# Kernel optimization log

Measured on AMD Instinct MI355X. Metric: run time of the kernel, lower is better.

## Reference

```python
import jax, jax.numpy as jnp
import numpy as np

B, S, D, H, DH, W, V, K = 2, 4096, 768, 12, 64, 128, 50265, 128
NEG = -1e9


def _ln(x, g, b, eps=1e-5):
    m = jnp.mean(x, axis=-1, keepdims=True)
    v = jnp.var(x, axis=-1, keepdims=True)
    return (x - m) * jax.lax.rsqrt(v + eps) * g + b


def _split_heads(x):  # [B,S,D] -> [B,H,S,DH]
    return x.reshape(B, S, H, DH).transpose(0, 2, 1, 3)


def _windows(xc):  # [B,H,C,W,DH] -> [B,H,C,3W,DH] (prev/self/next chunk)
    xp = jnp.pad(xc, ((0, 0), (0, 0), (1, 1), (0, 0), (0, 0)))
    return jnp.concatenate([xp[:, :, :-2], xp[:, :, 1:-1], xp[:, :, 2:]], axis=3)


def _forward(sentences, start_pieces, end_pieces, labels,
             emb, pos, ln0_g, ln0_b, wq, bq, wk, bk, wv, bv, wo, bo,
             ln1_g, ln1_b, w1, b1, w2, b2, ln2_g, ln2_b, exemplars):
    C = S // W
    scale = 1.0 / np.sqrt(DH)
    am = sentences != 1  # pad token id is 1 (mask = sentence_tokens != 1)
    gidx = jnp.concatenate([start_pieces, end_pieces], axis=1)  # [B,2] global tokens
    G = gidx.shape[1]

    # embeddings
    x = _ln(emb[sentences] + pos[None], ln0_g, ln0_b)  # [B,S,D]

    # --- Longformer layer: sliding-window + global attention ---
    q = _split_heads(x @ wq + bq)
    k = _split_heads(x @ wk + bk)
    v = _split_heads(x @ wv + bv)

    qc = q.reshape(B, H, C, W, DH)
    kw = _windows(k.reshape(B, H, C, W, DH))  # [B,H,C,3W,DH]
    vw = _windows(v.reshape(B, H, C, W, DH))

    # banded local scores
    sb = jnp.einsum('bhcqd,bhckd->bhcqk', qc, kw) * scale  # [B,H,C,W,3W]
    qi = jnp.arange(W)[:, None]
    kj = jnp.arange(3 * W)[None, :]
    band = jnp.abs(kj - W - qi) <= W  # [W,3W]
    amc = jnp.pad(am.reshape(B, C, W), ((0, 0), (1, 1), (0, 0)))
    amw = jnp.concatenate([amc[:, :-2], amc[:, 1:-1], amc[:, 2:]], axis=2)  # [B,C,3W]
    mask = band[None, None, None] & amw[:, None, :, None, :]
    sb = jnp.where(mask, sb, NEG).reshape(B, H, S, 3 * W)

    # every token also attends to the G global tokens
    gk = jnp.take_along_axis(k, gidx[:, None, :, None], axis=2)  # [B,H,G,DH]
    gv = jnp.take_along_axis(v, gidx[:, None, :, None], axis=2)
    sg = jnp.einsum('bhsd,bhgd->bhsg', q, gk) * scale  # [B,H,S,G]

    p = jax.nn.softmax(jnp.concatenate([sb, sg], axis=-1), axis=-1)
    pb = p[..., :3 * W].reshape(B, H, C, W, 3 * W)
    pg = p[..., 3 * W:]
    o = jnp.einsum('bhcqk,bhckd->bhcqd', pb, vw).reshape(B, H, S, DH)
    o = o + jnp.einsum('bhsg,bhgd->bhsd', pg, gv)

    # global query tokens attend to everything
    qg = jnp.take_along_axis(q, gidx[:, None, :, None], axis=2)  # [B,H,G,DH]
    sgq = jnp.einsum('bhgd,bhsd->bhgs', qg, k) * scale
    sgq = jnp.where(am[:, None, None, :], sgq, NEG)
    og = jnp.einsum('bhgs,bhsd->bhgd', jax.nn.softmax(sgq, axis=-1), v)

    o = o.transpose(0, 2, 1, 3).reshape(B, S, D)
    og = og.transpose(0, 2, 1, 3).reshape(B, G, D)
    o = o.at[jnp.arange(B)[:, None], gidx].set(og)

    x = _ln(x + (o @ wo + bo), ln1_g, ln1_b)
    ff = jax.nn.gelu(x @ w1 + b1, approximate=False) @ w2 + b2
    h = _ln(x + ff, ln2_g, ln2_b)  # last_hidden_state

    # mention reps: gather start & end piece vectors, concat -> [B, 2D]
    sv = jnp.take_along_axis(h, start_pieces[:, :, None], axis=1)[:, 0]
    ev = jnp.take_along_axis(h, end_pieces[:, :, None], axis=1)[:, 0]
    mention = jnp.concatenate([sv, ev], axis=-1)  # [B, 1536]

    logits = mention @ exemplars.T  # [B, K]
    logp = jax.nn.log_softmax(logits, axis=-1)
    loss = -jnp.sum(jnp.take_along_axis(logp, labels[:, None], axis=1))
    return logits, loss


def setup_inputs() -> dict:
    key = jax.random.key(0)
    ks = jax.random.split(key, 16)
    f = lambda k, s: (jax.random.normal(k, s, dtype=jnp.float32) * 0.02)
    return {
        'sentences': jax.random.randint(ks[0], (B, S), 0, V, dtype=jnp.int32),
        'start_pieces': jax.random.randint(ks[1], (B, 1), 0, S, dtype=jnp.int32),
        'end_pieces': jax.random.randint(ks[2], (B, 1), 0, S, dtype=jnp.int32),
        'labels': jax.random.randint(ks[3], (B,), 0, K, dtype=jnp.int32),
        'emb': f(ks[4], (V, D)), 'pos': f(ks[5], (S, D)),
        'ln0_g': jnp.ones(D), 'ln0_b': jnp.zeros(D),
        'wq': f(ks[6], (D, D)), 'bq': jnp.zeros(D),
        'wk': f(ks[7], (D, D)), 'bk': jnp.zeros(D),
        'wv': f(ks[8], (D, D)), 'bv': jnp.zeros(D),
        'wo': f(ks[9], (D, D)), 'bo': jnp.zeros(D),
        'ln1_g': jnp.ones(D), 'ln1_b': jnp.zeros(D),
        'w1': f(ks[10], (D, 4 * D)), 'b1': jnp.zeros(4 * D),
        'w2': f(ks[11], (4 * D, D)), 'b2': jnp.zeros(D),
        'ln2_g': jnp.ones(D), 'ln2_b': jnp.zeros(D),
        'exemplars': f(ks[12], (K, 2 * D)),
    }


def reference(sentences, start_pieces, end_pieces, labels,
              emb, pos, ln0_g, ln0_b, wq, bq, wk, bk, wv, bv, wo, bo,
              ln1_g, ln1_b, w1, b1, w2, b2, ln2_g, ln2_b, exemplars):
    return _forward(sentences, start_pieces, end_pieces, labels,
                    emb, pos, ln0_g, ln0_b, wq, bq, wk, bk, wv, bv, wo, bo,
                    ln1_g, ln1_b, w1, b1, w2, b2, ln2_g, ln2_b, exemplars)
```

## Files before the change

### kernel.cpp

```cpp
#include <hip/hip_runtime.h>

typedef unsigned short u16;
typedef unsigned int   u32;
typedef __attribute__((ext_vector_type(8))) short bf16x8;
typedef __attribute__((ext_vector_type(4))) float f32x4;

#define BB 2
#define SS 4096
#define DD 768
#define HH 12
#define FF 3072
#define NTOK 8192

#define GLDS16(gp, lp) __builtin_amdgcn_global_load_lds(                      \
    (const __attribute__((address_space(1))) u32*)(gp),                       \
    (__attribute__((address_space(3))) u32*)(lp), 16, 0, 0)

__device__ __forceinline__ float bf2f(u16 u) {
  return __uint_as_float(((u32)u) << 16);
}
__device__ __forceinline__ u16 f2bf(float f) {
  u32 x = __float_as_uint(f);
  x = x + 0x7FFFu + ((x >> 16) & 1u);
  return (u16)(x >> 16);
}
__device__ __forceinline__ float gelu_f(float v) {
  return 0.5f * v * (1.0f + erff(v * 0.70710678118654752f));
}

template<bool MAXOP>
__device__ __forceinline__ float blk_reduce(float v, float* sbuf) {
  #pragma unroll
  for (int o = 32; o > 0; o >>= 1) {
    float t = __shfl_xor(v, o, 64);
    v = MAXOP ? fmaxf(v, t) : (v + t);
  }
  int wave = threadIdx.x >> 6;
  int nw = blockDim.x >> 6;
  __syncthreads();
  if ((threadIdx.x & 63) == 0) sbuf[wave] = v;
  __syncthreads();
  float r = sbuf[0];
  for (int i = 1; i < nw; i++) r = MAXOP ? fmaxf(r, sbuf[i]) : (r + sbuf[i]);
  return r;
}

__global__ __launch_bounds__(256) void transcvt2(const float* __restrict__ wk,
    const float* __restrict__ wv, u16* __restrict__ wkT, u16* __restrict__ wvT,
    const int* sp, const int* ep, const float* bq, const float* bo,
    const float* b1, const float* b2,
    float* qg, float* oa, float* f1, float* f2, int* gidx) {
  int tid = threadIdx.x;
  if (blockIdx.x == 0 && blockIdx.y == 0 && blockIdx.z == 0) {
    if (tid < 4) {
      int b = tid >> 1;
      int s = (tid & 1) ? ep[b] : sp[b];
      gidx[tid] = b * SS + s;
    }
    for (int i = tid; i < DD; i += 256) {
      float vq = bq[i], vo = bo[i], v2 = b2[i];
      #pragma unroll
      for (int r = 0; r < 4; r++) {
        qg[r * DD + i] = vq; oa[r * DD + i] = vo; f2[r * DD + i] = v2;
      }
    }
    for (int i = tid; i < FF; i += 256) {
      float v1 = b1[i];
      #pragma unroll
      for (int r = 0; r < 4; r++) f1[r * FF + i] = v1;
    }
  }
  const float* W = blockIdx.z ? wv : wk;
  u16* WT = blockIdx.z ? wvT : wkT;
  __shared__ float t[32][33];
  int n0 = blockIdx.x * 32, k0 = blockIdx.y * 32;
  int tx = tid & 31, ty = tid >> 5;
  #pragma unroll
  for (int i = 0; i < 32; i += 8)
    t[ty + i][tx] = W[(size_t)(k0 + ty + i) * DD + n0 + tx];
  __syncthreads();
  #pragma unroll
  for (int i = 0; i < 32; i += 8)
    WT[(size_t)(n0 + ty + i) * DD + k0 + tx] = f2bf(t[tx][ty + i]);
}

__global__ __launch_bounds__(192) void embed_ln_k(const int* __restrict__ sent,
    const float* __restrict__ emb, const float* __restrict__ pos,
    const float* __restrict__ g, const float* __restrict__ be, u16* __restrict__ xout) {
  __shared__ float sbuf[8];
  int tok = blockIdx.x;
  int s = tok & (SS - 1);
  int row = sent[tok];
  int tid = threadIdx.x;
  float4 e = *(const float4*)(emb + (size_t)row * DD + tid * 4);
  float4 p = *(const float4*)(pos + (size_t)s * DD + tid * 4);
  float v0 = e.x + p.x, v1 = e.y + p.y, v2 = e.z + p.z, v3 = e.w + p.w;
  float sum = v0 + v1 + v2 + v3;
  float sq  = v0 * v0 + v1 * v1 + v2 * v2 + v3 * v3;
  sum = blk_reduce<false>(sum, sbuf);
  sq  = blk_reduce<false>(sq, sbuf);
  float mean = sum * (1.f / DD);
  float var  = sq * (1.f / DD) - mean * mean;
  float rstd = rsqrtf(var + 1e-5f);
  float4 gg = *(const float4*)(g + tid * 4);
  float4 bb = *(const float4*)(be + tid * 4);
  float o0 = (v0 - mean) * rstd * gg.x + bb.x;
  float o1 = (v1 - mean) * rstd * gg.y + bb.y;
  float o2 = (v2 - mean) * rstd * gg.z + bb.z;
  float o3 = (v3 - mean) * rstd * gg.w + bb.w;
  u32 lo = (u32)f2bf(o0) | ((u32)f2bf(o1) << 16);
  u32 hi = (u32)f2bf(o2) | ((u32)f2bf(o3) << 16);
  uint2 st; st.x = lo; st.y = hi;
  *(uint2*)(xout + (size_t)tok * DD + tid * 4) = st;
}

__global__ __launch_bounds__(256) void gemm_kv(const u16* __restrict__ A,
    const u16* __restrict__ wkT, const u16* __restrict__ wvT,
    const float* __restrict__ bkp, const float* __restrict__ bvp,
    u16* __restrict__ kb, u16* __restrict__ vb,
    const float* __restrict__ wqw, const int* __restrict__ gidx,
    float* __restrict__ qg) {
  __shared__ u16 As[128 * 32];
  __shared__ u16 Bs[128 * 32];
  __shared__ float s_in[4 * 64];
  int tid = threadIdx.x;
  if (blockIdx.y == 12) {
    if (blockIdx.x >= 36) return;
    int nc = blockIdx.x % 3, ky = blockIdx.x / 3;
    int rr = tid >> 6, kk0 = tid & 63;
    s_in[rr * 64 + kk0] = bf2f(A[(size_t)gidx[rr] * DD + ky * 64 + kk0]);
    __syncthreads();
    int n = nc * 256 + tid;
    int k0 = ky * 64;
    float a0 = 0.f, a1 = 0.f, a2 = 0.f, a3 = 0.f;
    for (int kk = 0; kk < 64; kk++) {
      float w = wqw[(size_t)(k0 + kk) * DD + n];
      a0 += s_in[kk] * w;
      a1 += s_in[64 + kk] * w;
      a2 += s_in[128 + kk] * w;
      a3 += s_in[192 + kk] * w;
    }
    atomicAdd(&qg[n], a0);
    atomicAdd(&qg[DD + n], a1);
    atomicAdd(&qg[2 * DD + n], a2);
    atomicAdd(&qg[3 * DD + n], a3);
    return;
  }
  const int K = DD, N = DD;
  int which = blockIdx.y >= 6;
  int m0 = blockIdx.x * 128;
  int n0 = (blockIdx.y - (which ? 6 : 0)) * 128;
  const u16* Bt = which ? wvT : wkT;
  const float* bias = which ? bvp : bkp;
  u16* C = which ? vb : kb;
  int lane = tid & 63, wave = tid >> 6;
  int wr = wave >> 1, wc = wave & 1;
  f32x4 acc[4][4] = {};
  int ch0 = wave * 64 + lane;
  int r0 = ch0 >> 2, su0 = ch0 & 3;
  int ch1 = 256 + ch0;
  int r1 = ch1 >> 2, su1 = ch1 & 3;
  const u16* a0p = A  + (size_t)(m0 + r0) * K + su0 * 8;
  const u16* a1p = A  + (size_t)(m0 + r1) * K + su1 * 8;
  const u16* b0p = Bt + (size_t)(n0 + r0) * K + su0 * 8;
  const u16* b1p = Bt + (size_t)(n0 + r1) * K + su1 * 8;
  u16* AsW0 = As + (size_t)(wave * 64) * 8;
  u16* AsW1 = As + (size_t)(256 + wave * 64) * 8;
  u16* BsW0 = Bs + (size_t)(wave * 64) * 8;
  u16* BsW1 = Bs + (size_t)(256 + wave * 64) * 8;
  int fr = lane & 15, fk = (lane >> 4) * 8;
  for (int k0 = 0; k0 < K; k0 += 32) {
    GLDS16(a0p + k0, AsW0);
    GLDS16(a1p + k0, AsW1);
    GLDS16(b0p + k0, BsW0);
    GLDS16(b1p + k0, BsW1);
    __syncthreads();
    bf16x8 af[4], bfr[4];
    #pragma unroll
    for (int i = 0; i < 4; i++)
      af[i] = *(const bf16x8*)(As + ((wr * 64 + i * 16 + fr) << 5) + fk);
    #pragma unroll
    for (int j = 0; j < 4; j++)
      bfr[j] = *(const bf16x8*)(Bs + ((wc * 64 + j * 16 + fr) << 5) + fk);
    #pragma unroll
    for (int i = 0; i < 4; i++)
      #pragma unroll
      for (int j = 0; j < 4; j++)
        acc[i][j] = __builtin_amdgcn_mfma_f32_16x16x32_bf16(af[i], bfr[j], acc[i][j], 0, 0, 0);
    __syncthreads();
  }
  int cr = (lane >> 4) * 4;
  int cc = lane & 15;
  #pragma unroll
  for (int i = 0; i < 4; i++) {
    #pragma unroll
    for (int j = 0; j < 4; j++) {
      int col = n0 + wc * 64 + j * 16 + cc;
      float bvv = bias[col];
      int rowb = m0 + wr * 64 + i * 16 + cr;
      #pragma unroll
      for (int r = 0; r < 4; r++) {
        float v = acc[i][j][r] + bvv;
        C[(size_t)(rowb + r) * N + col] = f2bf(v);
      }
    }
  }
}

__global__ __launch_bounds__(256) void gattn_part(const u16* __restrict__ kb,
    const u16* __restrict__ vb, const float* __restrict__ qg, const int* __restrict__ sent,
    float* __restrict__ part) {
  int sc = blockIdx.x, h = blockIdx.y, b = blockIdx.z;
  __shared__ float pbuf0[256], pbuf1[256];
  __shared__ float ovs0[32][64], ovs1[32][64];
  __shared__ float sbuf[8];
  int tid = threadIdx.x;
  int rsub = tid >> 3, csub = tid & 7;
  float qr0[8], qr1[8];
  #pragma unroll
  for (int j = 0; j < 8; j++) {
    qr0[j] = qg[(2 * b) * DD + h * 64 + csub * 8 + j];
    qr1[j] = qg[(2 * b + 1) * DD + h * 64 + csub * 8 + j];
  }
  size_t kbase = ((size_t)b * SS + sc * 256) * DD + h * 64 + csub * 8;
  #pragma unroll
  for (int pass = 0; pass < 8; pass++) {
    int rowi = pass * 32 + rsub;
    uint4 u = *(const uint4*)(kb + kbase + (size_t)rowi * DD);
    u32 vals[4] = {u.x, u.y, u.z, u.w};
    float d0 = 0.f, d1 = 0.f;
    #pragma unroll
    for (int t = 0; t < 4; t++) {
      float lo = __uint_as_float(vals[t] << 16);
      float hi = __uint_as_float(vals[t] & 0xFFFF0000u);
      d0 += qr0[t * 2] * lo + qr0[t * 2 + 1] * hi;
      d1 += qr1[t * 2] * lo + qr1[t * 2 + 1] * hi;
    }
    d0 += __shfl_xor(d0, 1, 64); d1 += __shfl_xor(d1, 1, 64);
    d0 += __shfl_xor(d0, 2, 64); d1 += __shfl_xor(d1, 2, 64);
    d0 += __shfl_xor(d0, 4, 64); d1 += __shfl_xor(d1, 4, 64);
    if (csub == 0) { pbuf0[rowi] = d0; pbuf1[rowi] = d1; }
  }
  __syncthreads();
  int ok = sent[b * SS + sc * 256 + tid] != 1;
  float s0 = ok ? pbuf0[tid] * 0.125f : -1e9f;
  float s1 = ok ? pbuf1[tid] * 0.125f : -1e9f;
  float m0 = blk_reduce<true>(s0, sbuf);
  float m1 = blk_reduce<true>(s1, sbuf);
  float p0 = expf(s0 - m0);
  float p1 = expf(s1 - m1);
  float ps0 = blk_reduce<false>(p0, sbuf);
  float ps1 = blk_reduce<false>(p1, sbuf);
  pbuf0[tid] = p0;
  pbuf1[tid] = p1;
  __syncthreads();
  float a0[8] = {0,0,0,0,0,0,0,0}, a1[8] = {0,0,0,0,0,0,0,0};
  #pragma unroll
  for (int pass = 0; pass < 8; pass++) {
    int rowi = pass * 32 + rsub;
    uint4 u = *(const uint4*)(vb + kbase + (size_t)rowi * DD);
    u32 vals[4] = {u.x, u.y, u.z, u.w};
    float pw0 = pbuf0[rowi], pw1 = pbuf1[rowi];
    #pragma unroll
    for (int t = 0; t < 4; t++) {
      float lo = __uint_as_float(vals[t] << 16);
      float hi = __uint_as_float(vals[t] & 0xFFFF0000u);
      a0[t * 2]     += pw0 * lo; a0[t * 2 + 1] += pw0 * hi;
      a1[t * 2]     += pw1 * lo; a1[t * 2 + 1] += pw1 * hi;
    }
  }
  #pragma unroll
  for (int j = 0; j < 8; j++) {
    ovs0[rsub][csub * 8 + j] = a0[j];
    ovs1[rsub][csub * 8 + j] = a1[j];
  }
  __syncthreads();
  float* pp0 = part + (((size_t)(2 * b) * HH + h) * 16 + sc) * 66;
  float* pp1 = part + (((size_t)(2 * b + 1) * HH + h) * 16 + sc) * 66;
  if (tid == 0) { pp0[0] = m0; pp0[1] = ps0; pp1[0] = m1; pp1[1] = ps1; }
  if (tid < 64) {
    float o0 = 0.f, o1 = 0.f;
    #pragma unroll
    for (int g2 = 0; g2 < 32; g2++) { o0 += ovs0[g2][tid]; o1 += ovs1[g2][tid]; }
    pp0[2 + tid] = o0;
    pp1[2 + tid] = o1;
  }
}

__global__ __launch_bounds__(256) void matvec_wo(const float* __restrict__ W,
    const float* __restrict__ part, float* __restrict__ acc) {
  __shared__ float s_in[4][64];
  int h = blockIdx.y;
  int tid = threadIdx.x;
  int bg = tid >> 6, d = tid & 63;
  const float* pp = part + (((size_t)bg * HH + h) * 16) * 66;
  float M = -1e30f;
  for (int c = 0; c < 16; c++) M = fmaxf(M, pp[c * 66]);
  float Ssum = 0.f, o = 0.f;
  for (int c = 0; c < 16; c++) {
    float e = expf(pp[c * 66] - M);
    Ssum += pp[c * 66 + 1] * e;
    o += pp[c * 66 + 2 + d] * e;
  }
  s_in[bg][d] = o / Ssum;
  __syncthreads();
  int n = blockIdx.x * 256 + tid;
  int k0 = h * 64;
  float a0 = 0.f, a1 = 0.f, a2 = 0.f, a3 = 0.f;
  for (int kk = 0; kk < 64; kk++) {
    float w = W[(size_t)(k0 + kk) * DD + n];
    a0 += s_in[0][kk] * w;
    a1 += s_in[1][kk] * w;
    a2 += s_in[2][kk] * w;
    a3 += s_in[3][kk] * w;
  }
  atomicAdd(&acc[n], a0);
  atomicAdd(&acc[DD + n], a1);
  atomicAdd(&acc[2 * DD + n], a2);
  atomicAdd(&acc[3 * DD + n], a3);
}

__global__ __launch_bounds__(256) void w1ln_k(const u16* __restrict__ xb,
    const int* __restrict__ gidx, const float* __restrict__ oacc,
    const float* __restrict__ g1, const float* __restrict__ be1,
    float* __restrict__ x1, const float* __restrict__ w1, float* __restrict__ f1a) {
  __shared__ float sbuf[8];
  __shared__ float xr[4][DD];
  int tid = threadIdx.x;
  for (int r = 0; r < 4; r++) {
    float v[3]; float sum = 0.f, sq = 0.f;
    #pragma unroll
    for (int i = 0; i < 3; i++) {
      int d = tid + i * 256;
      float t = bf2f(xb[(size_t)gidx[r] * DD + d]) + oacc[r * DD + d];
      v[i] = t; sum += t; sq += t * t;
    }
    sum = blk_reduce<false>(sum, sbuf);
    sq  = blk_reduce<false>(sq, sbuf);
    float mean = sum * (1.f / DD);
    float rstd = rsqrtf(sq * (1.f / DD) - mean * mean + 1e-5f);
    #pragma unroll
    for (int i = 0; i < 3; i++) {
      int d = tid + i * 256;
      xr[r][d] = (v[i] - mean) * rstd * g1[d] + be1[d];
    }
  }
  __syncthreads();
  if (blockIdx.x == 0 && blockIdx.y == 0) {
    for (int r = 0; r < 4; r++)
      #pragma unroll
      for (int i = 0; i < 3; i++) {
        int d = tid + i * 256;
        x1[r * DD + d] = xr[r][d];
      }
  }
  int k0 = blockIdx.y * 48;
  int n = blockIdx.x * 256 + tid;
  float a0 = 0.f, a1 = 0.f, a2 = 0.f, a3 = 0.f;
  for (int kk = 0; kk < 48; kk++) {
    float w = w1[(size_t)(k0 + kk) * FF + n];
    a0 += xr[0][k0 + kk] * w; a1 += xr[1][k0 + kk] * w;
    a2 += xr[2][k0 + kk] * w; a3 += xr[3][k0 + kk] * w;
  }
  atomicAdd(&f1a[n], a0);
  atomicAdd(&f1a[FF + n], a1);
  atomicAdd(&f1a[2 * FF + n], a2);
  atomicAdd(&f1a[3 * FF + n], a3);
}

__global__ __launch_bounds__(256) void w2_k(const float* __restrict__ f1a,
    const float* __restrict__ w2, float* __restrict__ f2a) {
  __shared__ float sI[4][48];
  int tid = threadIdx.x;
  int k0 = blockIdx.y * 48;
  for (int idx = tid; idx < 192; idx += 256) {
    int r = idx / 48, kk = idx % 48;
    sI[r][kk] = gelu_f(f1a[(size_t)r * FF + k0 + kk]);
  }
  __syncthreads();
  int n = blockIdx.x * 256 + tid;
  float a0 = 0.f, a1 = 0.f, a2 = 0.f, a3 = 0.f;
  for (int kk = 0; kk < 48; kk++) {
    float w = w2[(size_t)(k0 + kk) * DD + n];
    a0 += sI[0][kk] * w; a1 += sI[1][kk] * w;
    a2 += sI[2][kk] * w; a3 += sI[3][kk] * w;
  }
  atomicAdd(&f2a[n], a0);
  atomicAdd(&f2a[DD + n], a1);
  atomicAdd(&f2a[2 * DD + n], a2);
  atomicAdd(&f2a[3 * DD + n], a3);
}

__global__ __launch_bounds__(256) void logits_k(const float* __restrict__ x1,
    const float* __restrict__ f2a, const float* __restrict__ g2,
    const float* __restrict__ be2, const float* __restrict__ ex,
    float* __restrict__ out) {
  __shared__ float sbuf[8];
  __shared__ float hw[4][DD];
  int tid = threadIdx.x;
  for (int r = 0; r < 4; r++) {
    float v[3]; float sum = 0.f, sq = 0.f;
    #pragma unroll
    for (int i = 0; i < 3; i++) {
      int d = tid + i * 256;
      float t = x1[r * DD + d] + f2a[r * DD + d];
      v[i] = t; sum += t; sq += t * t;
    }
    sum = blk_reduce<false>(sum, sbuf);
    sq  = blk_reduce<false>(sq, sbuf);
    float mean = sum * (1.f / DD);
    float rstd = rsqrtf(sq * (1.f / DD) - mean * mean + 1e-5f);
    #pragma unroll
    for (int i = 0; i < 3; i++) {
      int d = tid + i * 256;
      hw[r][d] = (v[i] - mean) * rstd * g2[d] + be2[d];
    }
  }
  __syncthreads();
  int j = blockIdx.x;
  const float* er = ex + (size_t)j * 1536;
  float d0 = 0.f, d1 = 0.f;
  for (int c = tid; c < DD; c += 256) {
    float e0 = er[c], e1 = er[DD + c];
    d0 += hw[0][c] * e0 + hw[1][c] * e1;
    d1 += hw[2][c] * e0 + hw[3][c] * e1;
  }
  d0 = blk_reduce<false>(d0, sbuf);
  d1 = blk_reduce<false>(d1, sbuf);
  if (tid == 0) { out[j] = d0; out[128 + j] = d1; }
}

__global__ __launch_bounds__(128) void loss_k(const float* __restrict__ lg,
    const int* __restrict__ labels, float* __restrict__ out) {
  __shared__ float sbuf[8];
  int tid = threadIdx.x;
  float v0 = lg[tid], v1 = lg[128 + tid];
  float m0 = blk_reduce<true>(v0, sbuf);
  float m1 = blk_reduce<true>(v1, sbuf);
  float s0 = blk_reduce<false>(expf(v0 - m0), sbuf);
  float s1 = blk_reduce<false>(expf(v1 - m1), sbuf);
  if (tid == 0) {
    float lp0 = lg[labels[0]] - m0 - logf(s0);
    float lp1 = lg[128 + labels[1]] - m1 - logf(s1);
    out[256] = -(lp0 + lp1);
  }
}

extern "C" void kernel_launch(void* const* d_in, const int* in_sizes, int n_in,
                              void* d_out, int out_size, void* d_ws, size_t ws_size,
                              hipStream_t stream) {
  const int*   sent = (const int*)d_in[0];
  const int*   sp   = (const int*)d_in[1];
  const int*   ep   = (const int*)d_in[2];
  const int*   lab  = (const int*)d_in[3];
  const float* emb  = (const float*)d_in[4];
  const float* pos  = (const float*)d_in[5];
  const float* ln0g = (const float*)d_in[6];
  const float* ln0b = (const float*)d_in[7];
  const float* wq   = (const float*)d_in[8];
  const float* bq   = (const float*)d_in[9];
  const float* wk   = (const float*)d_in[10];
  const float* bk   = (const float*)d_in[11];
  const float* wv   = (const float*)d_in[12];
  const float* bv   = (const float*)d_in[13];
  const float* wo   = (const float*)d_in[14];
  const float* bo   = (const float*)d_in[15];
  const float* ln1g = (const float*)d_in[16];
  const float* ln1b = (const float*)d_in[17];
  const float* w1   = (const float*)d_in[18];
  const float* b1   = (const float*)d_in[19];
  const float* w2   = (const float*)d_in[20];
  const float* b2   = (const float*)d_in[21];
  const float* ln2g = (const float*)d_in[22];
  const float* ln2b = (const float*)d_in[23];
  const float* ex   = (const float*)d_in[24];
  float* out = (float*)d_out;

  char* basep = (char*)d_ws;
  size_t off = 0;
  auto alloc = [&](size_t bytes) -> void* {
    void* p = basep + off;
    off = (off + bytes + 255) & ~(size_t)255;
    return p;
  };
  u16*   xb   = (u16*)alloc((size_t)NTOK * DD * 2);
  u16*   kb   = (u16*)alloc((size_t)NTOK * DD * 2);
  u16*   vb   = (u16*)alloc((size_t)NTOK * DD * 2);
  u16*   wkT  = (u16*)alloc((size_t)DD * DD * 2);
  u16*   wvT  = (u16*)alloc((size_t)DD * DD * 2);
  float* qg   = (float*)alloc(4 * DD * 4);
  float* oacc = (float*)alloc(4 * DD * 4);
  float* x1   = (float*)alloc(4 * DD * 4);
  float* f1a  = (float*)alloc(4 * FF * 4);
  float* f2a  = (float*)alloc(4 * DD * 4);
  float* part = (float*)alloc((size_t)4 * HH * 16 * 66 * 4);
  int*   gidx = (int*)alloc(64);

  transcvt2<<<dim3(24, 24, 2), 256, 0, stream>>>(wk, wv, wkT, wvT,
      sp, ep, bq, bo, b1, b2, qg, oacc, f1a, f2a, gidx);
  embed_ln_k<<<NTOK, 192, 0, stream>>>(sent, emb, pos, ln0g, ln0b, xb);
  gemm_kv<<<dim3(64, 13), 256, 0, stream>>>(xb, wkT, wvT, bk, bv, kb, vb, wq, gidx, qg);
  gattn_part<<<dim3(16, HH, 2), 256, 0, stream>>>(kb, vb, qg, sent, part);
  matvec_wo<<<dim3(3, HH), 256, 0, stream>>>(wo, part, oacc);
  w1ln_k<<<dim3(12, 16), 256, 0, stream>>>(xb, gidx, oacc, ln1g, ln1b, x1, w1, f1a);
  w2_k<<<dim3(3, 64), 256, 0, stream>>>(f1a, w2, f2a);
  logits_k<<<128, 256, 0, stream>>>(x1, f2a, ln2g, ln2b, ex, out);
  loss_k<<<1, 128, 0, stream>>>(out, lab, out);
}
```

Measured before the change: 105.5 us.

## Merge weight transpose into embed kernel and deepen GEMM K-tile to 64

The separate weight-transpose/bias-init kernel is folded into the embedding+LayerNorm launch as extra blocks appended after the token blocks, which removes one kernel launch and its serialization point. Independently, the K/V projection GEMM now stages a 64-wide K slice per iteration instead of 32, which halves the number of barrier pairs and loop iterations at the cost of doubling LDS per block. The transpose blocks now run with 192 threads, so row coverage is guarded, and the LDS reads use a 64-element row stride that may cause more bank conflicts.

```diff
diff --git a/kernel.cpp b/kernel.cpp
--- a/kernel.cpp
+++ b/kernel.cpp
@@ -45,53 +45,63 @@
   return r;
 }
 
-__global__ __launch_bounds__(256) void transcvt2(const float* __restrict__ wk,
-    const float* __restrict__ wv, u16* __restrict__ wkT, u16* __restrict__ wvT,
+__global__ __launch_bounds__(192) void embed_ln_k(const int* __restrict__ sent,
+    const float* __restrict__ emb, const float* __restrict__ pos,
+    const float* __restrict__ g, const float* __restrict__ be, u16* __restrict__ xout,
+    const float* __restrict__ wk, const float* __restrict__ wv,
+    u16* __restrict__ wkT, u16* __restrict__ wvT,
     const int* sp, const int* ep, const float* bq, const float* bo,
     const float* b1, const float* b2,
     float* qg, float* oa, float* f1, float* f2, int* gidx) {
   int tid = threadIdx.x;
-  if (blockIdx.x == 0 && blockIdx.y == 0 && blockIdx.z == 0) {
-    if (tid < 4) {
-      int b = tid >> 1;
-      int s = (tid & 1) ? ep[b] : sp[b];
-      gidx[tid] = b * SS + s;
-    }
-    for (int i = tid; i < DD; i += 256) {
-      float vq = bq[i], vo = bo[i], v2 = b2[i];
-      #pragma unroll
-      for (int r = 0; r < 4; r++) {
-        qg[r * DD + i] = vq; oa[r * DD + i] = vo; f2[r * DD + i] = v2;
+  int bid = blockIdx.x;
+  if (bid >= NTOK) {
+    int t = bid - NTOK;
+    if (t == 0) {
+      if (tid < 4) {
+        int b = tid >> 1;
+        int s = (tid & 1) ? ep[b] : sp[b];
+        gidx[tid] = b * SS + s;
       }
-    }
-    for (int i = tid; i < FF; i += 256) {
-      float v1 = b1[i];
-      #pragma unroll
-      for (int r = 0; r < 4; r++) f1[r * FF + i] = v1;
-    }
-  }
-  const float* W = blockIdx.z ? wv : wk;
-  u16* WT = blockIdx.z ? wvT : wkT;
-  __shared__ float t[32][33];
-  int n0 = blockIdx.x * 32, k0 = blockIdx.y * 32;
-  int tx = tid & 31, ty = tid >> 5;
-  #pragma unroll
-  for (int i = 0; i < 32; i += 8)
-    t[ty + i][tx] = W[(size_t)(k0 + ty + i) * DD + n0 + tx];
-  __syncthreads();
-  #pragma unroll
-  for (int i = 0; i < 32; i += 8)
-    WT[(size_t)(n0 + ty + i) * DD + k0 + tx] = f2bf(t[tx][ty + i]);
-}
-
-__global__ __launch_bounds__(192) void embed_ln_k(const int* __restrict__ sent,
-    const float* __restrict__ emb, const float* __restrict__ pos,
-    const float* __restrict__ g, const float* __restrict__ be, u16* __restrict__ xout) {
+      for (int i = tid; i < DD; i += 192) {
+        float vq = bq[i], vo = bo[i], v2 = b2[i];
+        #pragma unroll
+        for (int r = 0; r < 4; r++) {
+          qg[r * DD + i] = vq; oa[r * DD + i] = vo; f2[r * DD + i] = v2;
+        }
+      }
+      for (int i = tid; i < FF; i += 192) {
+        float v1 = b1[i];
+        #pragma unroll
+        for (int r = 0; r < 4; r++) f1[r * FF + i] = v1;
+      }
+    }
+    int z = t >= 576;
+    int tt = z ? t - 576 : t;
+    const float* W = z ? wv : wk;
+    u16* WT = z ? wvT : wkT;
+    __shared__ float tld[32][33];
+    int n0 = (tt % 24) * 32, k0 = (tt / 24) * 32;
+    int tx = tid & 31, ty = tid >> 5;
+    #pragma unroll
+    for (int i = 0; i < 6; i++) {
+      int row = ty + i * 6;
+      if (row < 32)
+        tld[row][tx] = W[(size_t)(k0 + row) * DD + n0 + tx];
+    }
+    __syncthreads();
+    #pragma unroll
+    for (int i = 0; i < 6; i++) {
+      int row = ty + i * 6;
+      if (row < 32)
+        WT[(size_t)(n0 + row) * DD + k0 + tx] = f2bf(tld[tx][row]);
+    }
+    return;
+  }
   __shared__ float sbuf[8];
-  int tok = blockIdx.x;
+  int tok = bid;
   int s = tok & (SS - 1);
   int row = sent[tok];
-  int tid = threadIdx.x;
   float4 e = *(const float4*)(emb + (size_t)row * DD + tid * 4);
   float4 p = *(const float4*)(pos + (size_t)s * DD + tid * 4);
   float v0 = e.x + p.x, v1 = e.y + p.y, v2 = e.z + p.z, v3 = e.w + p.w;
@@ -120,8 +130,8 @@
     u16* __restrict__ kb, u16* __restrict__ vb,
     const float* __restrict__ wqw, const int* __restrict__ gidx,
     float* __restrict__ qg) {
-  __shared__ u16 As[128 * 32];
-  __shared__ u16 Bs[128 * 32];
+  __shared__ u16 As[128 * 64];
+  __shared__ u16 Bs[128 * 64];
   __shared__ float s_in[4 * 64];
   int tid = threadIdx.x;
   if (blockIdx.y == 12) {
@@ -156,37 +166,40 @@
   int lane = tid & 63, wave = tid >> 6;
   int wr = wave >> 1, wc = wave & 1;
   f32x4 acc[4][4] = {};
-  int ch0 = wave * 64 + lane;
-  int r0 = ch0 >> 2, su0 = ch0 & 3;
-  int ch1 = 256 + ch0;
-  int r1 = ch1 >> 2, su1 = ch1 & 3;
-  const u16* a0p = A  + (size_t)(m0 + r0) * K + su0 * 8;
-  const u16* a1p = A  + (size_t)(m0 + r1) * K + su1 * 8;
-  const u16* b0p = Bt + (size_t)(n0 + r0) * K + su0 * 8;
-  const u16* b1p = Bt + (size_t)(n0 + r1) * K + su1 * 8;
-  u16* AsW0 = As + (size_t)(wave * 64) * 8;
-  u16* AsW1 = As + (size_t)(256 + wave * 64) * 8;
-  u16* BsW0 = Bs + (size_t)(wave * 64) * 8;
-  u16* BsW1 = Bs + (size_t)(256 + wave * 64) * 8;
+  const u16* ap[4]; const u16* bp[4];
+  u16* AsW[4]; u16* BsW[4];
+  #pragma unroll
+  for (int q = 0; q < 4; q++) {
+    int ch = q * 256 + tid;
+    int rr = ch >> 3, su = ch & 7;
+    ap[q] = A  + (size_t)(m0 + rr) * K + su * 8;
+    bp[q] = Bt + (size_t)(n0 + rr) * K + su * 8;
+    AsW[q] = As + (size_t)(q * 256 + wave * 64) * 8;
+    BsW[q] = Bs + (size_t)(q * 256 + wave * 64) * 8;
+  }
   int fr = lane & 15, fk = (lane >> 4) * 8;
-  for (int k0 = 0; k0 < K; k0 += 32) {
-    GLDS16(a0p + k0, AsW0);
-    GLDS16(a1p + k0, AsW1);
-    GLDS16(b0p + k0, BsW0);
-    GLDS16(b1p + k0, BsW1);
+  for (int k0 = 0; k0 < K; k0 += 64) {
+    #pragma unroll
+    for (int q = 0; q < 4; q++) {
+      GLDS16(ap[q] + k0, AsW[q]);
+      GLDS16(bp[q] + k0, BsW[q]);
+    }
     __syncthreads();
-    bf16x8 af[4], bfr[4];
-    #pragma unroll
-    for (int i = 0; i < 4; i++)
-      af[i] = *(const bf16x8*)(As + ((wr * 64 + i * 16 + fr) << 5) + fk);
-    #pragma unroll
-    for (int j = 0; j < 4; j++)
-      bfr[j] = *(const bf16x8*)(Bs + ((wc * 64 + j * 16 + fr) << 5) + fk);
-    #pragma unroll
-    for (int i = 0; i < 4; i++)
+    #pragma unroll
+    for (int ks = 0; ks < 64; ks += 32) {
+      bf16x8 af[4], bfr[4];
+      #pragma unroll
+      for (int i = 0; i < 4; i++)
+        af[i] = *(const bf16x8*)(As + ((wr * 64 + i * 16 + fr) << 6) + ks + fk);
       #pragma unroll
       for (int j = 0; j < 4; j++)
-        acc[i][j] = __builtin_amdgcn_mfma_f32_16x16x32_bf16(af[i], bfr[j], acc[i][j], 0, 0, 0);
+        bfr[j] = *(const bf16x8*)(Bs + ((wc * 64 + j * 16 + fr) << 6) + ks + fk);
+      #pragma unroll
+      for (int i = 0; i < 4; i++)
+        #pragma unroll
+        for (int j = 0; j < 4; j++)
+          acc[i][j] = __builtin_amdgcn_mfma_f32_16x16x32_bf16(af[i], bfr[j], acc[i][j], 0, 0, 0);
+    }
     __syncthreads();
   }
   int cr = (lane >> 4) * 4;
@@ -496,9 +509,8 @@
   float* part = (float*)alloc((size_t)4 * HH * 16 * 66 * 4);
   int*   gidx = (int*)alloc(64);
 
-  transcvt2<<<dim3(24, 24, 2), 256, 0, stream>>>(wk, wv, wkT, wvT,
-      sp, ep, bq, bo, b1, b2, qg, oacc, f1a, f2a, gidx);
-  embed_ln_k<<<NTOK, 192, 0, stream>>>(sent, emb, pos, ln0g, ln0b, xb);
+  embed_ln_k<<<NTOK + 1152, 192, 0, stream>>>(sent, emb, pos, ln0g, ln0b, xb,
+      wk, wv, wkT, wvT, sp, ep, bq, bo, b1, b2, qg, oacc, f1a, f2a, gidx);
   gemm_kv<<<dim3(64, 13), 256, 0, stream>>>(xb, wkT, wvT, bk, bv, kb, vb, wq, gidx, qg);
   gattn_part<<<dim3(16, HH, 2), 256, 0, stream>>>(kb, vb, qg, sent, part);
   matvec_wo<<<dim3(3, HH), 256, 0, stream>>>(wo, part, oacc);
```

Result: slower. 108.8 us (+3.1%).
